# Optimization experiments

Measured on AMD Instinct MI355X. Metric: run time of the kernel, lower is better.

Reference implementation:

```python
import jax, jax.numpy as jnp
import numpy as np

B, DIN, NS, NF = 2048, 512, 256, 64

def setup_inputs() -> dict:
    key = jax.random.key(0)
    ks = jax.random.split(key, 16)
    s = 0.05
    return {
        'x_i': jax.random.normal(ks[0], (B, DIN), jnp.float32),
        'h_i': jax.random.normal(ks[1], (B, NS), jnp.float32),
        'S_i': jax.random.normal(ks[2], (B, 2, NS, NF), jnp.float32),
        'W_fste': jax.random.normal(ks[3], (DIN + NS, NS), jnp.float32) * s,
        'b_fste': jnp.zeros((NS,), jnp.float32),
        'W_ffreq': jax.random.normal(ks[4], (DIN + NS, NF), jnp.float32) * s,
        'b_ffreq': jnp.zeros((NF,), jnp.float32),
        'W_i': jax.random.normal(ks[5], (DIN + NS, NS), jnp.float32) * s,
        'b_i': jnp.zeros((NS,), jnp.float32),
        'W_c': jax.random.normal(ks[6], (DIN + NS, NS), jnp.float32) * s,
        'b_c': jnp.zeros((NS,), jnp.float32),
        'u_a': jax.random.normal(ks[7], (NF,), jnp.float32) * s,
        'b_a': jnp.zeros((NS,), jnp.float32),
        'W_o': jax.random.normal(ks[8], (DIN + NS + NS, NS), jnp.float32) * s,
        'b_o': jnp.zeros((NS,), jnp.float32),
        't': 3,
    }

def reference(x_i, h_i, S_i, W_fste, b_fste, W_ffreq, b_ffreq, W_i, b_i, W_c, b_c, u_a, b_a, W_o, b_o, t):
    nf = u_a.shape[0]
    # angle = ((arange(nf)*t) % nf) / (nf / (2*pi))  -- matches np precedence in source
    ang = ((jnp.arange(nf, dtype=jnp.float32) * t) % nf) * (2.0 * jnp.pi / nf)
    omega = jnp.stack([jnp.sin(ang), jnp.cos(ang)])[:, None]        # [2,1,nf]
    x_h = jnp.concatenate([x_i, h_i], axis=-1)                      # [B, DIN+NS]
    f_ste = jax.nn.sigmoid(x_h @ W_fste + b_fste)                   # [B,NS]
    f_freq = jax.nn.sigmoid(x_h @ W_ffreq + b_ffreq)                # [B,NF]
    F_t = jnp.einsum('bi,bj->bij', f_ste, f_freq)                   # [B,NS,NF]
    i_dot = jax.nn.sigmoid(x_h @ W_i + b_i)                         # [B,NS]
    c_wave = jnp.tanh(x_h @ W_c + b_c)                              # [B,NS]
    i_c_omega = (i_dot * c_wave)[:, None, :, None] * omega          # [B,2,NS,NF]
    S_next = S_i * F_t[:, None] + i_c_omega                         # [B,2,NS,NF]
    A_i = jnp.sqrt(jnp.sum(S_next ** 2, axis=1))                    # [B,NS,NF]
    c_t = jax.nn.sigmoid(jnp.einsum('bij,j->bi', A_i, u_a) + b_a)   # [B,NS]
    o_i = jax.nn.sigmoid(jnp.concatenate([x_h, c_t], -1) @ W_o + b_o)
    h_next = o_i * c_t
    return h_next, S_next
```

## Files before the change

kernel.cpp:

```cpp
#include <hip/hip_runtime.h>
#include <math.h>

#define BATCH 2048
#define DIN   512
#define NS    256
#define NF    64
#define KG    768
#define NG    832
#define KO    1024

__device__ __forceinline__ float sigmoidf_(float x) { return 1.0f / (1.0f + __expf(-x)); }

__global__ __launch_bounds__(256) void gates_gemm(
    const float* __restrict__ x, const float* __restrict__ h,
    const float* __restrict__ Wf, const float* __restrict__ bf,
    const float* __restrict__ Wq, const float* __restrict__ bq,
    const float* __restrict__ Wi, const float* __restrict__ bi,
    const float* __restrict__ Wc, const float* __restrict__ bcg,
    float* __restrict__ gates)
{
    __shared__ float As[16][68];
    __shared__ float Bs[16][68];

    const int nt = blockIdx.x;
    const int mt = blockIdx.y;
    const int t  = threadIdx.x;

    const int n0 = nt * 64;
    const float* Wp; const float* bp; int ld, noff, act;
    if (n0 < 256)      { Wp = Wf; bp = bf;  ld = 256; noff = 0;   act = 0; }
    else if (n0 < 320) { Wp = Wq; bp = bq;  ld = 64;  noff = 256; act = 0; }
    else if (n0 < 576) { Wp = Wi; bp = bi;  ld = 256; noff = 320; act = 0; }
    else               { Wp = Wc; bp = bcg; ld = 256; noff = 576; act = 1; }
    const int nloc0 = n0 - noff;

    const int tx = t & 15, ty = t >> 4;
    const int m0 = mt * 64;

    const int ar = t >> 2;
    const int ak = (t & 3) * 4;
    const int bk   = t >> 4;
    const int bcol = (t & 15) * 4;

    float acc[4][4] = {};

    for (int kt = 0; kt < KG; kt += 16) {
        {
            const int k = kt + ak;
            const int m = m0 + ar;
            float4 a4 = (k < DIN) ? *(const float4*)(x + (size_t)m * DIN + k)
                                  : *(const float4*)(h + (size_t)m * NS + (k - DIN));
            As[ak + 0][ar] = a4.x; As[ak + 1][ar] = a4.y;
            As[ak + 2][ar] = a4.z; As[ak + 3][ar] = a4.w;
        }
        *(float4*)&Bs[bk][bcol] = *(const float4*)(Wp + (size_t)(kt + bk) * ld + nloc0 + bcol);
        __syncthreads();

        #pragma unroll
        for (int kk = 0; kk < 16; ++kk) {
            float4 a = *(const float4*)&As[kk][ty * 4];
            float4 b = *(const float4*)&Bs[kk][tx * 4];
            float av[4] = { a.x, a.y, a.z, a.w };
            float bv[4] = { b.x, b.y, b.z, b.w };
            #pragma unroll
            for (int r = 0; r < 4; ++r)
                #pragma unroll
                for (int c = 0; c < 4; ++c)
                    acc[r][c] = fmaf(av[r], bv[c], acc[r][c]);
        }
        __syncthreads();
    }

    const float4 bb = *(const float4*)(bp + nloc0 + tx * 4);
    const float bvv[4] = { bb.x, bb.y, bb.z, bb.w };
    #pragma unroll
    for (int r = 0; r < 4; ++r) {
        const int m = m0 + ty * 4 + r;
        #pragma unroll
        for (int c = 0; c < 4; ++c) {
            float v = acc[r][c] + bvv[c];
            v = act ? tanhf(v) : sigmoidf_(v);
            gates[(size_t)m * NG + n0 + tx * 4 + c] = v;
        }
    }
}

__global__ __launch_bounds__(256) void supdate(
    const float* __restrict__ S, const float* __restrict__ gates,
    const float* __restrict__ ua, const float* __restrict__ ba,
    const int* __restrict__ tptr,
    float* __restrict__ Sout, float* __restrict__ ct)
{
    const int tid = blockIdx.x * 256 + threadIdx.x;
    const int q    = tid & 15;
    const int pair = tid >> 4;
    const int b = pair >> 8, s = pair & 255;
    const int f0 = q * 4;
    const int tv = *tptr;

    const float* grow = gates + (size_t)b * NG;
    const float fste = grow[s];
    const float ic   = grow[320 + s] * grow[576 + s];

    const float4 ff  = *(const float4*)(grow + 256 + f0);
    const float4 ua4 = *(const float4*)(ua + f0);

    const size_t base0 = (((size_t)b * 2 + 0) * NS + s) * NF + f0;
    const size_t base1 = (((size_t)b * 2 + 1) * NS + s) * NF + f0;
    const float4 si0 = *(const float4*)(S + base0);
    const float4 si1 = *(const float4*)(S + base1);

    float fv[4] = { ff.x, ff.y, ff.z, ff.w };
    float uv[4] = { ua4.x, ua4.y, ua4.z, ua4.w };
    float a0[4] = { si0.x, si0.y, si0.z, si0.w };
    float a1[4] = { si1.x, si1.y, si1.z, si1.w };

    float part = 0.0f;
    float o0[4], o1[4];
    #pragma unroll
    for (int j = 0; j < 4; ++j) {
        int f = f0 + j;
        float ang = (float)((f * tv) & (NF - 1)) * (float)(M_PI / 32.0);
        float sn = __sinf(ang), cs = __cosf(ang);
        float F = fste * fv[j];
        float u = a0[j] * F + ic * sn;
        float v = a1[j] * F + ic * cs;
        o0[j] = u; o1[j] = v;
        part += sqrtf(u * u + v * v) * uv[j];
    }
    *(float4*)(Sout + base0) = make_float4(o0[0], o0[1], o0[2], o0[3]);
    *(float4*)(Sout + base1) = make_float4(o1[0], o1[1], o1[2], o1[3]);

    part += __shfl_xor(part, 1);
    part += __shfl_xor(part, 2);
    part += __shfl_xor(part, 4);
    part += __shfl_xor(part, 8);
    if (q == 0) ct[pair] = sigmoidf_(part + ba[s]);
}

__global__ __launch_bounds__(256) void out_gemm(
    const float* __restrict__ x, const float* __restrict__ h,
    const float* __restrict__ ct,
    const float* __restrict__ Wo, const float* __restrict__ bo,
    float* __restrict__ hout)
{
    __shared__ float As[16][68];
    __shared__ float Bs[16][68];

    const int nt = blockIdx.x;
    const int mt = blockIdx.y;
    const int t  = threadIdx.x;
    const int n0 = nt * 64;
    const int tx = t & 15, ty = t >> 4;
    const int m0 = mt * 64;

    const int ar = t >> 2;
    const int ak = (t & 3) * 4;
    const int bk   = t >> 4;
    const int bcol = (t & 15) * 4;

    float acc[4][4] = {};

    for (int kt = 0; kt < KO; kt += 16) {
        {
            const int k = kt + ak;
            const int m = m0 + ar;
            float4 a4;
            if (k < DIN)           a4 = *(const float4*)(x  + (size_t)m * DIN + k);
            else if (k < DIN + NS) a4 = *(const float4*)(h  + (size_t)m * NS + (k - DIN));
            else                   a4 = *(const float4*)(ct + (size_t)m * NS + (k - DIN - NS));
            As[ak + 0][ar] = a4.x; As[ak + 1][ar] = a4.y;
            As[ak + 2][ar] = a4.z; As[ak + 3][ar] = a4.w;
        }
        *(float4*)&Bs[bk][bcol] = *(const float4*)(Wo + (size_t)(kt + bk) * NS + n0 + bcol);
        __syncthreads();

        #pragma unroll
        for (int kk = 0; kk < 16; ++kk) {
            float4 a = *(const float4*)&As[kk][ty * 4];
            float4 b = *(const float4*)&Bs[kk][tx * 4];
            float av[4] = { a.x, a.y, a.z, a.w };
            float bv[4] = { b.x, b.y, b.z, b.w };
            #pragma unroll
            for (int r = 0; r < 4; ++r)
                #pragma unroll
                for (int c = 0; c < 4; ++c)
                    acc[r][c] = fmaf(av[r], bv[c], acc[r][c]);
        }
        __syncthreads();
    }

    #pragma unroll
    for (int r = 0; r < 4; ++r) {
        const int m = m0 + ty * 4 + r;
        #pragma unroll
        for (int c = 0; c < 4; ++c) {
            const int n = n0 + tx * 4 + c;
            float o = sigmoidf_(acc[r][c] + bo[n]);
            hout[(size_t)m * NS + n] = o * ct[(size_t)m * NS + n];
        }
    }
}

extern "C" void kernel_launch(void* const* d_in, const int* in_sizes, int n_in,
                              void* d_out, int out_size, void* d_ws, size_t ws_size,
                              hipStream_t stream)
{
    const float* x  = (const float*)d_in[0];
    const float* h  = (const float*)d_in[1];
    const float* S  = (const float*)d_in[2];
    const float* Wf = (const float*)d_in[3];
    const float* bf = (const float*)d_in[4];
    const float* Wq = (const float*)d_in[5];
    const float* bq = (const float*)d_in[6];
    const float* Wi = (const float*)d_in[7];
    const float* bi = (const float*)d_in[8];
    const float* Wc = (const float*)d_in[9];
    const float* bc = (const float*)d_in[10];
    const float* ua = (const float*)d_in[11];
    const float* ba = (const float*)d_in[12];
    const float* Wo = (const float*)d_in[13];
    const float* bo = (const float*)d_in[14];
    const int*   tp = (const int*)d_in[15];

    float* gates = (float*)d_ws;
    float* ct    = gates + (size_t)BATCH * NG;
    float* hout  = (float*)d_out;
    float* Sout  = hout + (size_t)BATCH * NS;

    gates_gemm<<<dim3(13, 32), 256, 0, stream>>>(x, h, Wf, bf, Wq, bq, Wi, bi, Wc, bc, gates);
    supdate<<<dim3((BATCH * NS * 16) / 256), 256, 0, stream>>>(S, gates, ua, ba, tp, Sout, ct);
    out_gemm<<<dim3(4, 32), 256, 0, stream>>>(x, h, ct, Wo, bo, hout);
}
```

Baseline: 601.3 us.

## Fold x_h part of output GEMM into gates GEMM and double-buffer tiles

The output projection is split so the x_h-dependent part (first 768 rows of W_o) is computed inside the gates GEMM as four extra N-tiles and stored as a partial sum. The out GEMM then only reduces over the 256 c_t columns and uses smaller M tiles for more blocks. Both GEMMs move to K=32 tiles with register-prefetched double-buffered shared memory. This costs an extra workspace buffer and larger shared-memory use per block.

```diff
diff --git a/kernel.cpp b/kernel.cpp
--- a/kernel.cpp
+++ b/kernel.cpp
@@ -7,7 +7,7 @@
 #define NF    64
 #define KG    768
 #define NG    832
-#define KO    1024
+#define NTOT  1088
 
 __device__ __forceinline__ float sigmoidf_(float x) { return 1.0f / (1.0f + __expf(-x)); }
 
@@ -17,10 +17,11 @@
     const float* __restrict__ Wq, const float* __restrict__ bq,
     const float* __restrict__ Wi, const float* __restrict__ bi,
     const float* __restrict__ Wc, const float* __restrict__ bcg,
-    float* __restrict__ gates)
+    const float* __restrict__ Wo,
+    float* __restrict__ gates, float* __restrict__ opart)
 {
-    __shared__ float As[16][68];
-    __shared__ float Bs[16][68];
+    __shared__ float As[2][32][68];
+    __shared__ float Bs[2][32][68];
 
     const int nt = blockIdx.x;
     const int mt = blockIdx.y;
@@ -31,56 +32,100 @@
     if (n0 < 256)      { Wp = Wf; bp = bf;  ld = 256; noff = 0;   act = 0; }
     else if (n0 < 320) { Wp = Wq; bp = bq;  ld = 64;  noff = 256; act = 0; }
     else if (n0 < 576) { Wp = Wi; bp = bi;  ld = 256; noff = 320; act = 0; }
-    else               { Wp = Wc; bp = bcg; ld = 256; noff = 576; act = 1; }
+    else if (n0 < 832) { Wp = Wc; bp = bcg; ld = 256; noff = 576; act = 1; }
+    else               { Wp = Wo; bp = bf;  ld = 256; noff = 832; act = 2; }
     const int nloc0 = n0 - noff;
 
     const int tx = t & 15, ty = t >> 4;
     const int m0 = mt * 64;
 
-    const int ar = t >> 2;
-    const int ak = (t & 3) * 4;
-    const int bk   = t >> 4;
-    const int bcol = (t & 15) * 4;
+    const int ar  = t & 63;
+    const int ak0 = (t >> 6) * 8;
+    const int brow  = t >> 3;
+    const int bcol0 = (t & 7) * 8;
+
+    const float* ax = x + (size_t)(m0 + ar) * DIN;
+    const float* ah = h + (size_t)(m0 + ar) * NS;
 
     float acc[4][4] = {};
-
-    for (int kt = 0; kt < KG; kt += 16) {
-        {
-            const int k = kt + ak;
-            const int m = m0 + ar;
-            float4 a4 = (k < DIN) ? *(const float4*)(x + (size_t)m * DIN + k)
-                                  : *(const float4*)(h + (size_t)m * NS + (k - DIN));
-            As[ak + 0][ar] = a4.x; As[ak + 1][ar] = a4.y;
-            As[ak + 2][ar] = a4.z; As[ak + 3][ar] = a4.w;
-        }
-        *(float4*)&Bs[bk][bcol] = *(const float4*)(Wp + (size_t)(kt + bk) * ld + nloc0 + bcol);
-        __syncthreads();
-
+    float4 a0, a1, b0, b1;
+
+    {
+        const int k0 = ak0;
+        a0 = *(const float4*)(ax + k0);
+        a1 = *(const float4*)(ax + k0 + 4);
+        const float* wr = Wp + (size_t)brow * ld + nloc0 + bcol0;
+        b0 = *(const float4*)wr; b1 = *(const float4*)(wr + 4);
+        As[0][ak0 + 0][ar] = a0.x; As[0][ak0 + 1][ar] = a0.y;
+        As[0][ak0 + 2][ar] = a0.z; As[0][ak0 + 3][ar] = a0.w;
+        As[0][ak0 + 4][ar] = a1.x; As[0][ak0 + 5][ar] = a1.y;
+        As[0][ak0 + 6][ar] = a1.z; As[0][ak0 + 7][ar] = a1.w;
+        *(float4*)&Bs[0][brow][bcol0]     = b0;
+        *(float4*)&Bs[0][brow][bcol0 + 4] = b1;
+    }
+    __syncthreads();
+
+    #pragma unroll 1
+    for (int tI = 0; tI < 24; ++tI) {
+        const int notlast = (tI < 23);
+        if (notlast) {
+            const int kt = (tI + 1) * 32;
+            const int k0 = kt + ak0;
+            a0 = (k0 < DIN)     ? *(const float4*)(ax + k0)
+                                : *(const float4*)(ah + (k0 - DIN));
+            a1 = (k0 + 4 < DIN) ? *(const float4*)(ax + k0 + 4)
+                                : *(const float4*)(ah + (k0 + 4 - DIN));
+            const float* wr = Wp + (size_t)(kt + brow) * ld + nloc0 + bcol0;
+            b0 = *(const float4*)wr; b1 = *(const float4*)(wr + 4);
+        }
+        const float (*Asb)[68] = As[tI & 1];
+        const float (*Bsb)[68] = Bs[tI & 1];
         #pragma unroll
-        for (int kk = 0; kk < 16; ++kk) {
-            float4 a = *(const float4*)&As[kk][ty * 4];
-            float4 b = *(const float4*)&Bs[kk][tx * 4];
-            float av[4] = { a.x, a.y, a.z, a.w };
-            float bv[4] = { b.x, b.y, b.z, b.w };
+        for (int kk = 0; kk < 32; ++kk) {
+            const float4 a = *(const float4*)&Asb[kk][ty * 4];
+            const float4 b = *(const float4*)&Bsb[kk][tx * 4];
+            const float av[4] = { a.x, a.y, a.z, a.w };
+            const float bv[4] = { b.x, b.y, b.z, b.w };
             #pragma unroll
             for (int r = 0; r < 4; ++r)
                 #pragma unroll
                 for (int c = 0; c < 4; ++c)
                     acc[r][c] = fmaf(av[r], bv[c], acc[r][c]);
         }
+        if (notlast) {
+            float (*Ad)[68] = As[(tI + 1) & 1];
+            float (*Bd)[68] = Bs[(tI + 1) & 1];
+            Ad[ak0 + 0][ar] = a0.x; Ad[ak0 + 1][ar] = a0.y;
+            Ad[ak0 + 2][ar] = a0.z; Ad[ak0 + 3][ar] = a0.w;
+            Ad[ak0 + 4][ar] = a1.x; Ad[ak0 + 5][ar] = a1.y;
+            Ad[ak0 + 6][ar] = a1.z; Ad[ak0 + 7][ar] = a1.w;
+            *(float4*)&Bd[brow][bcol0]     = b0;
+            *(float4*)&Bd[brow][bcol0 + 4] = b1;
+        }
         __syncthreads();
     }
 
-    const float4 bb = *(const float4*)(bp + nloc0 + tx * 4);
-    const float bvv[4] = { bb.x, bb.y, bb.z, bb.w };
-    #pragma unroll
-    for (int r = 0; r < 4; ++r) {
-        const int m = m0 + ty * 4 + r;
+    if (act == 2) {
         #pragma unroll
-        for (int c = 0; c < 4; ++c) {
-            float v = acc[r][c] + bvv[c];
-            v = act ? tanhf(v) : sigmoidf_(v);
-            gates[(size_t)m * NG + n0 + tx * 4 + c] = v;
+        for (int r = 0; r < 4; ++r) {
+            const int m = m0 + ty * 4 + r;
+            *(float4*)(opart + (size_t)m * NS + (n0 - 832) + tx * 4) =
+                make_float4(acc[r][0], acc[r][1], acc[r][2], acc[r][3]);
+        }
+    } else {
+        const float4 bb = *(const float4*)(bp + nloc0 + tx * 4);
+        const float bvv[4] = { bb.x, bb.y, bb.z, bb.w };
+        #pragma unroll
+        for (int r = 0; r < 4; ++r) {
+            const int m = m0 + ty * 4 + r;
+            float o[4];
+            #pragma unroll
+            for (int c = 0; c < 4; ++c) {
+                float v = acc[r][c] + bvv[c];
+                o[c] = act ? tanhf(v) : sigmoidf_(v);
+            }
+            *(float4*)(gates + (size_t)m * NG + n0 + tx * 4) =
+                make_float4(o[0], o[1], o[2], o[3]);
         }
     }
 }
@@ -139,66 +184,88 @@
 }
 
 __global__ __launch_bounds__(256) void out_gemm(
-    const float* __restrict__ x, const float* __restrict__ h,
-    const float* __restrict__ ct,
+    const float* __restrict__ ct, const float* __restrict__ opart,
     const float* __restrict__ Wo, const float* __restrict__ bo,
     float* __restrict__ hout)
 {
-    __shared__ float As[16][68];
-    __shared__ float Bs[16][68];
-
-    const int nt = blockIdx.x;
-    const int mt = blockIdx.y;
+    __shared__ float As[2][32][36];
+    __shared__ float Bs[2][32][68];
+
     const int t  = threadIdx.x;
-    const int n0 = nt * 64;
+    const int n0 = blockIdx.x * 64;
+    const int m0 = blockIdx.y * 32;
     const int tx = t & 15, ty = t >> 4;
-    const int m0 = mt * 64;
-
-    const int ar = t >> 2;
-    const int ak = (t & 3) * 4;
-    const int bk   = t >> 4;
-    const int bcol = (t & 15) * 4;
-
-    float acc[4][4] = {};
-
-    for (int kt = 0; kt < KO; kt += 16) {
-        {
-            const int k = kt + ak;
-            const int m = m0 + ar;
-            float4 a4;
-            if (k < DIN)           a4 = *(const float4*)(x  + (size_t)m * DIN + k);
-            else if (k < DIN + NS) a4 = *(const float4*)(h  + (size_t)m * NS + (k - DIN));
-            else                   a4 = *(const float4*)(ct + (size_t)m * NS + (k - DIN - NS));
-            As[ak + 0][ar] = a4.x; As[ak + 1][ar] = a4.y;
-            As[ak + 2][ar] = a4.z; As[ak + 3][ar] = a4.w;
-        }
-        *(float4*)&Bs[bk][bcol] = *(const float4*)(Wo + (size_t)(kt + bk) * NS + n0 + bcol);
+
+    const int ar  = t & 31;
+    const int ak0 = (t >> 5) * 4;
+    const int brow  = t >> 3;
+    const int bcol0 = (t & 7) * 8;
+
+    const float* Wp = Wo + (size_t)(DIN + NS) * NS;
+    const float* act_row = ct + (size_t)(m0 + ar) * NS;
+
+    float acc[2][4] = {};
+    float4 a4, b0, b1;
+
+    a4 = *(const float4*)(act_row + ak0);
+    {
+        const float* wr = Wp + (size_t)brow * NS + n0 + bcol0;
+        b0 = *(const float4*)wr; b1 = *(const float4*)(wr + 4);
+    }
+    As[0][ak0 + 0][ar] = a4.x; As[0][ak0 + 1][ar] = a4.y;
+    As[0][ak0 + 2][ar] = a4.z; As[0][ak0 + 3][ar] = a4.w;
+    *(float4*)&Bs[0][brow][bcol0]     = b0;
+    *(float4*)&Bs[0][brow][bcol0 + 4] = b1;
+    __syncthreads();
+
+    #pragma unroll 1
+    for (int tI = 0; tI < 8; ++tI) {
+        const int notlast = (tI < 7);
+        if (notlast) {
+            const int kt = (tI + 1) * 32;
+            a4 = *(const float4*)(act_row + kt + ak0);
+            const float* wr = Wp + (size_t)(kt + brow) * NS + n0 + bcol0;
+            b0 = *(const float4*)wr; b1 = *(const float4*)(wr + 4);
+        }
+        const float (*Asb)[36] = As[tI & 1];
+        const float (*Bsb)[68] = Bs[tI & 1];
+        #pragma unroll
+        for (int kk = 0; kk < 32; ++kk) {
+            const float a0v = Asb[kk][ty * 2];
+            const float a1v = Asb[kk][ty * 2 + 1];
+            const float4 b = *(const float4*)&Bsb[kk][tx * 4];
+            acc[0][0] = fmaf(a0v, b.x, acc[0][0]);
+            acc[0][1] = fmaf(a0v, b.y, acc[0][1]);
+            acc[0][2] = fmaf(a0v, b.z, acc[0][2]);
+            acc[0][3] = fmaf(a0v, b.w, acc[0][3]);
+            acc[1][0] = fmaf(a1v, b.x, acc[1][0]);
+            acc[1][1] = fmaf(a1v, b.y, acc[1][1]);
+            acc[1][2] = fmaf(a1v, b.z, acc[1][2]);
+            acc[1][3] = fmaf(a1v, b.w, acc[1][3]);
+        }
+        if (notlast) {
+            float (*Ad)[36] = As[(tI + 1) & 1];
+            float (*Bd)[68] = Bs[(tI + 1) & 1];
+            Ad[ak0 + 0][ar] = a4.x; Ad[ak0 + 1][ar] = a4.y;
+            Ad[ak0 + 2][ar] = a4.z; Ad[ak0 + 3][ar] = a4.w;
+            *(float4*)&Bd[brow][bcol0]     = b0;
+            *(float4*)&Bd[brow][bcol0 + 4] = b1;
+        }
         __syncthreads();
-
-        #pragma unroll
-        for (int kk = 0; kk < 16; ++kk) {
-            float4 a = *(const float4*)&As[kk][ty * 4];
-            float4 b = *(const float4*)&Bs[kk][tx * 4];
-            float av[4] = { a.x, a.y, a.z, a.w };
-            float bv[4] = { b.x, b.y, b.z, b.w };
-            #pragma unroll
-            for (int r = 0; r < 4; ++r)
-                #pragma unroll
-                for (int c = 0; c < 4; ++c)
-                    acc[r][c] = fmaf(av[r], bv[c], acc[r][c]);
-        }
-        __syncthreads();
     }
 
     #pragma unroll
-    for (int r = 0; r < 4; ++r) {
-        const int m = m0 + ty * 4 + r;
-        #pragma unroll
-        for (int c = 0; c < 4; ++c) {
-            const int n = n0 + tx * 4 + c;
-            float o = sigmoidf_(acc[r][c] + bo[n]);
-            hout[(size_t)m * NS + n] = o * ct[(size_t)m * NS + n];
-        }
+    for (int r = 0; r < 2; ++r) {
+        const int m = m0 + ty * 2 + r;
+        const float4 op = *(const float4*)(opart + (size_t)m * NS + n0 + tx * 4);
+        const float4 bb = *(const float4*)(bo + n0 + tx * 4);
+        const float4 cv = *(const float4*)(ct + (size_t)m * NS + n0 + tx * 4);
+        float4 o;
+        o.x = sigmoidf_(acc[r][0] + op.x + bb.x) * cv.x;
+        o.y = sigmoidf_(acc[r][1] + op.y + bb.y) * cv.y;
+        o.z = sigmoidf_(acc[r][2] + op.z + bb.z) * cv.z;
+        o.w = sigmoidf_(acc[r][3] + op.w + bb.w) * cv.w;
+        *(float4*)(hout + (size_t)m * NS + n0 + tx * 4) = o;
     }
 }
 
@@ -225,10 +292,11 @@
 
     float* gates = (float*)d_ws;
     float* ct    = gates + (size_t)BATCH * NG;
+    float* opart = ct + (size_t)BATCH * NS;
     float* hout  = (float*)d_out;
     float* Sout  = hout + (size_t)BATCH * NS;
 
-    gates_gemm<<<dim3(13, 32), 256, 0, stream>>>(x, h, Wf, bf, Wq, bq, Wi, bi, Wc, bc, gates);
+    gates_gemm<<<dim3(17, 32), 256, 0, stream>>>(x, h, Wf, bf, Wq, bq, Wi, bi, Wc, bc, Wo, gates, opart);
     supdate<<<dim3((BATCH * NS * 16) / 256), 256, 0, stream>>>(S, gates, ua, ba, tp, Sout, ct);
-    out_gemm<<<dim3(4, 32), 256, 0, stream>>>(x, h, ct, Wo, bo, hout);
+    out_gemm<<<dim3(4, 64), 256, 0, stream>>>(ct, opart, Wo, bo, hout);
 }
```

Result: no change. 594.1 us (-1.2%).
